# Kernel optimization log

Hardware: AMD Instinct MI355X
Metric: run time of the kernel (lower is better)

The kernel has to match this reference:

```python
import jax, jax.numpy as jnp
import numpy as np

B, V, L, C, H = 2, 8, 256, 1024, 16

def setup_inputs() -> dict:
    key = jax.random.key(0)
    ks = jax.random.split(key, 6)
    s = 0.02  # init scale for weights
    x = jax.random.normal(ks[0], (B, V, L, C), jnp.float32)
    Wq = jax.random.normal(ks[1], (C, C), jnp.float32) * s
    Wk = jax.random.normal(ks[2], (C, C), jnp.float32) * s
    Wv = jax.random.normal(ks[3], (C, C), jnp.float32) * s
    Wp = jax.random.normal(ks[4], (C, C), jnp.float32) * s
    bp = jnp.zeros((C,), jnp.float32)
    return {"x": x, "Wq": Wq, "Wk": Wk, "Wv": Wv, "Wp": Wp, "bp": bp}

def _view_mask(V, L):
    # view-level allow mask, expanded to token level [S, S]
    vi = jnp.arange(V)
    qv, kv = vi[:, None], vi[None, :]
    cross = ((qv == 0) & (kv == 1)) | ((qv == 1) & (kv == 0))
    later = (qv > 1) | (kv > 1)
    allow = cross | (later & (qv >= kv))  # [V, V]
    return jnp.repeat(jnp.repeat(allow, L, axis=0), L, axis=1)  # [V*L, V*L]

def reference(x, Wq, Wk, Wv, Wp, bp):
    b, v, l, c = x.shape
    h = H
    dh = c // h
    scale = dh ** -0.5
    s = v * l
    xf = x.reshape(b, s, c)
    # torch Linear: y = x @ W.T
    q = (xf @ Wq.T).reshape(b, s, h, dh).transpose(0, 2, 1, 3)  # [b,h,s,dh]
    k = (xf @ Wk.T).reshape(b, s, h, dh).transpose(0, 2, 1, 3)
    vv = (xf @ Wv.T).reshape(b, s, h, dh).transpose(0, 2, 1, 3)
    scores = jnp.einsum('bhqd,bhkd->bhqk', q, k) * scale  # [b,h,s,s]
    mask = _view_mask(v, l)
    scores = jnp.where(mask, scores, -jnp.inf)
    attn = jax.nn.softmax(scores, axis=-1)
    out = jnp.einsum('bhqk,bhkd->bhqd', attn, vv)
    out = out.transpose(0, 2, 1, 3).reshape(b, v, l, c)
    return out @ Wp.T + bp
```

## Files before the change

kernel.cpp:

```cpp
#include <hip/hip_runtime.h>
#include <stdint.h>

typedef unsigned short ushort_t;
typedef __attribute__((ext_vector_type(8))) __bf16 bf16x8;
typedef __attribute__((ext_vector_type(4))) float floatx4;
typedef __attribute__((ext_vector_type(2))) uint32_t uint32x2;

__device__ __forceinline__ ushort_t f2bf(float f) {
    uint32_t u = __builtin_bit_cast(uint32_t, f);
    u += 0x7fffu + ((u >> 16) & 1u);
    return (ushort_t)(u >> 16);
}

typedef __attribute__((address_space(1))) const void glb_void;
typedef __attribute__((address_space(3))) void lds_void;
__device__ __forceinline__ void gld16(const void* g, void* l) {
    __builtin_amdgcn_global_load_lds((glb_void*)g, (lds_void*)l, 16, 0, 0);
}

#define QSCALE 0.18033688011112042f

__global__ void cast_kernel(const float* __restrict__ x,
                            const float* __restrict__ Wq, const float* __restrict__ Wk,
                            const float* __restrict__ Wv, const float* __restrict__ Wp,
                            ushort_t* __restrict__ xb, ushort_t* __restrict__ Wqkvb,
                            ushort_t* __restrict__ Wpb)
{
    const int64_t NX = 4194304, NW = 1048576;
    int64_t i4 = ((int64_t)blockIdx.x * blockDim.x + threadIdx.x) * 4;
    const float* src; ushort_t* dst; int64_t off;
    if (i4 < NX)            { src = x;  dst = xb;          off = i4; }
    else if (i4 < NX+NW)    { src = Wq; dst = Wqkvb;       off = i4 - NX; }
    else if (i4 < NX+2*NW)  { src = Wk; dst = Wqkvb + NW;  off = i4 - NX - NW; }
    else if (i4 < NX+3*NW)  { src = Wv; dst = Wqkvb + 2*NW;off = i4 - NX - 2*NW; }
    else                    { src = Wp; dst = Wpb;         off = i4 - NX - 3*NW; }
    float4 v = *(const float4*)(src + off);
    ushort4 o;
    o.x = f2bf(v.x); o.y = f2bf(v.y); o.z = f2bf(v.z); o.w = f2bf(v.w);
    *(ushort4*)(dst + off) = o;
}

template<int BM, int BN, int BK, int MODE>
__global__ __launch_bounds__(256, 3)
void gemm_bt(const ushort_t* __restrict__ A, const ushort_t* __restrict__ Bmat,
             int M, int N, int K,
             ushort_t* __restrict__ qb, ushort_t* __restrict__ kb, ushort_t* __restrict__ vtb,
             float* __restrict__ outf, const float* __restrict__ bias)
{
    constexpr int KB32 = BK / 32;
    constexpr int NA = (BM / 16) * KB32;
    constexpr int NB = (BN / 16) * KB32;
    constexpr int NS = (NA + NB) / 4;
    constexpr int MT = BM / 32;
    constexpr int NTW = BN / 32;
    __shared__ ushort_t As[BM * BK];
    __shared__ ushort_t Bs[BN * BK];
    const int tid  = threadIdx.x;
    const int lane = tid & 63;
    const int wave = tid >> 6;
    const int m0 = blockIdx.x * BM;
    const int n0 = blockIdx.y * BN;
    const int wrow = (wave >> 1) * (BM / 2);
    const int wcol = (wave & 1) * (BN / 2);
    const int q_ = lane >> 4;
    const int ml = lane & 15;
    (void)M;

    floatx4 acc[MT][NTW];
    #pragma unroll
    for (int i = 0; i < MT; i++)
        #pragma unroll
        for (int j = 0; j < NTW; j++) acc[i][j] = floatx4{0.f,0.f,0.f,0.f};

    const int row_l = lane >> 2;
    const int col_l = (lane & 3) * 8;
    const ushort_t* gptr[NS];
    ushort_t* lptr[NS];
    #pragma unroll
    for (int i = 0; i < NS; i++) {
        int id = wave * NS + i;
        if (id < NA) {
            int rg = id / KB32, ch = id % KB32;
            gptr[i] = A + (int64_t)(m0 + rg*16 + row_l) * K + ch*32 + col_l;
            lptr[i] = As + id * 512;
        } else {
            int id2 = id - NA;
            int rg = id2 / KB32, ch = id2 % KB32;
            gptr[i] = Bmat + (int64_t)(n0 + rg*16 + row_l) * K + ch*32 + col_l;
            lptr[i] = Bs + id2 * 512;
        }
    }

    for (int k0 = 0; k0 < K; k0 += BK) {
        __syncthreads();
        #pragma unroll
        for (int i = 0; i < NS; i++) gld16(gptr[i] + k0, lptr[i]);
        __syncthreads();
        #pragma unroll
        for (int kk = 0; kk < KB32; kk++) {
            bf16x8 af[MT], bf[NTW];
            #pragma unroll
            for (int mt = 0; mt < MT; mt++)
                af[mt] = *(const bf16x8*)(As + ((wrow/16 + mt)*KB32 + kk)*512 + ml*32 + q_*8);
            #pragma unroll
            for (int nt = 0; nt < NTW; nt++)
                bf[nt] = *(const bf16x8*)(Bs + ((wcol/16 + nt)*KB32 + kk)*512 + ml*32 + q_*8);
            #pragma unroll
            for (int mt = 0; mt < MT; mt++)
                #pragma unroll
                for (int nt = 0; nt < NTW; nt++)
                    acc[mt][nt] = __builtin_amdgcn_mfma_f32_16x16x32_bf16(af[mt], bf[nt], acc[mt][nt], 0, 0, 0);
        }
    }

    if (MODE == 0) {
        #pragma unroll
        for (int mt = 0; mt < MT; mt++)
            #pragma unroll
            for (int nt = 0; nt < NTW; nt++) {
                floatx4 v = acc[mt][nt];
                int col = n0 + wcol + nt*16 + ml;
                int which = col >> 10;
                int nn = col & 1023;
                int h = nn >> 6, d = nn & 63;
                if (which < 2) {
                    ushort_t* dst = (which == 0) ? qb : kb;
                    float sc = (which == 0) ? QSCALE : 1.0f;
                    for (int r = 0; r < 4; r++) {
                        int rowg = m0 + wrow + mt*16 + q_*4 + r;
                        int b = rowg >> 11, s = rowg & 2047;
                        dst[(((int64_t)(b*16 + h) * 2048 + s) << 6) + d] = f2bf(v[r] * sc);
                    }
                } else {
                    int rowg0 = m0 + wrow + mt*16 + q_*4;
                    int b = rowg0 >> 11, sbase = rowg0 & 2047;
                    ushort4 o;
                    o.x = f2bf(v[0]); o.y = f2bf(v[1]); o.z = f2bf(v[2]); o.w = f2bf(v[3]);
                    *(ushort4*)(vtb + (((int64_t)(b*16 + h) * 64 + d) << 11) + sbase) = o;
                }
            }
    } else {
        #pragma unroll
        for (int mt = 0; mt < MT; mt++)
            #pragma unroll
            for (int nt = 0; nt < NTW; nt++) {
                floatx4 v = acc[mt][nt];
                int col = n0 + wcol + nt*16 + ml;
                float bv = bias[col];
                for (int r = 0; r < 4; r++) {
                    int rowg = m0 + wrow + mt*16 + q_*4 + r;
                    outf[(int64_t)rowg * N + col] = v[r] + bv;
                }
            }
    }
}

__global__ __launch_bounds__(256, 3)
void attn_kernel(const ushort_t* __restrict__ Q, const ushort_t* __restrict__ Kb,
                 const ushort_t* __restrict__ Vt, ushort_t* __restrict__ Out)
{
    __shared__ ushort_t Kl[8192];
    __shared__ ushort_t Vl[8192];
    __shared__ ushort_t Pl[4 * 16 * 136];

    int bi = blockIdx.x;
    int bh = (bi & 7) + 8 * ((bi >> 3) & 3);
    int qt = (bi >> 5) & 3;
    int qv = 7 - (bi >> 7);
    int b = bh >> 4, h = bh & 15;
    int tid = threadIdx.x;
    int wave = tid >> 6, lane = tid & 63;
    int q_ = lane >> 4, ml = lane & 15;
    int rlane = lane & 15, clane = lane >> 4;
    int s0 = qv*256 + qt*64 + wave*16;

    const ushort_t* Kbh = Kb + ((int64_t)bh << 17);
    const ushort_t* Vbh = Vt + ((int64_t)bh << 17);
    ushort_t* Pw = Pl + wave * (16 * 136);

    const ushort_t* Qp = Q + (((int64_t)bh*2048 + s0 + ml) << 6) + q_*8;
    bf16x8 aq0 = *(const bf16x8*)(Qp);
    bf16x8 aq1 = *(const bf16x8*)(Qp + 32);

    floatx4 o_acc[4];
    for (int i = 0; i < 4; i++) o_acc[i] = floatx4{0.f,0.f,0.f,0.f};
    float lsum = 0.f;

    const int nviews = (qv < 2) ? 1 : (qv + 1);
    const int vfix = qv ^ 1;

    for (int vi = 0; vi < nviews; vi++) {
        int kb0 = ((nviews == 1) ? vfix : vi) * 256;
        for (int ck = 0; ck < 2; ck++) {
            int koff = kb0 + ck * 128;

            __syncthreads();
            #pragma unroll
            for (int i = 0; i < 4; i++) {
                int id = wave*4 + i;
                const ushort_t* gk = Kbh + (((int64_t)(koff + (id >> 1)*16 + rlane)) << 6)
                                         + (id & 1)*32 + clane*8;
                gld16(gk, Kl + id*512);
                const ushort_t* gv = Vbh + ((int64_t)((id & 3)*16 + rlane) << 11)
                                         + koff + (id >> 2)*32 + clane*8;
                gld16(gv, Vl + id*512);
            }
            __syncthreads();

            #pragma unroll
            for (int kt = 0; kt < 8; kt++) {
                bf16x8 k0 = *(const bf16x8*)(Kl + kt*1024 + lane*8);
                bf16x8 k1 = *(const bf16x8*)(Kl + kt*1024 + 512 + lane*8);
                floatx4 cz = floatx4{0.f,0.f,0.f,0.f};
                cz = __builtin_amdgcn_mfma_f32_16x16x32_bf16(k0, aq0, cz, 0, 0, 0);
                cz = __builtin_amdgcn_mfma_f32_16x16x32_bf16(k1, aq1, cz, 0, 0, 0);

                float p0 = __builtin_amdgcn_exp2f(cz[0]);
                float p1 = __builtin_amdgcn_exp2f(cz[1]);
                float p2 = __builtin_amdgcn_exp2f(cz[2]);
                float p3 = __builtin_amdgcn_exp2f(cz[3]);
                lsum += (p0 + p1) + (p2 + p3);
                uint32x2 wv;
                wv[0] = (uint32_t)f2bf(p0) | ((uint32_t)f2bf(p1) << 16);
                wv[1] = (uint32_t)f2bf(p2) | ((uint32_t)f2bf(p3) << 16);
                *(uint32x2*)(Pw + ml*136 + kt*16 + q_*4) = wv;
            }

            asm volatile("s_waitcnt lgkmcnt(0)" ::: "memory");

            #pragma unroll
            for (int g = 0; g < 4; g++) {
                bf16x8 ap = *(const bf16x8*)(Pw + ml*136 + g*32 + q_*8);
                #pragma unroll
                for (int dt = 0; dt < 4; dt++) {
                    bf16x8 vv = *(const bf16x8*)(Vl + (g*4 + dt)*512 + lane*8);
                    o_acc[dt] = __builtin_amdgcn_mfma_f32_16x16x32_bf16(ap, vv, o_acc[dt], 0, 0, 0);
                }
            }
        }
    }

    lsum += __shfl_xor(lsum, 16);
    lsum += __shfl_xor(lsum, 32);
    float rinv[4];
    #pragma unroll
    for (int r = 0; r < 4; r++)
        rinv[r] = 1.0f / __shfl(lsum, q_*4 + r);

    #pragma unroll
    for (int dt = 0; dt < 4; dt++)
        #pragma unroll
        for (int r = 0; r < 4; r++) {
            float v = o_acc[dt][r] * rinv[r];
            int sr = s0 + q_*4 + r;
            Out[((int64_t)b*2048 + sr) * 1024 + h*64 + dt*16 + ml] = f2bf(v);
        }
}

extern "C" void kernel_launch(void* const* d_in, const int* in_sizes, int n_in,
                              void* d_out, int out_size, void* d_ws, size_t ws_size,
                              hipStream_t stream) {
    const float* x  = (const float*)d_in[0];
    const float* Wq = (const float*)d_in[1];
    const float* Wk = (const float*)d_in[2];
    const float* Wv = (const float*)d_in[3];
    const float* Wp = (const float*)d_in[4];
    const float* bp = (const float*)d_in[5];
    float* out = (float*)d_out;

    char* ws = (char*)d_ws;
    ushort_t* xb    = (ushort_t*)(ws);
    ushort_t* Wqkvb = (ushort_t*)(ws + ((size_t)8  << 20));
    ushort_t* Wpb   = (ushort_t*)(ws + ((size_t)14 << 20));
    ushort_t* qb    = (ushort_t*)(ws + ((size_t)16 << 20));
    ushort_t* kbuf  = (ushort_t*)(ws + ((size_t)24 << 20));
    ushort_t* vtb   = (ushort_t*)(ws + ((size_t)40 << 20));
    ushort_t* attno = xb;

    cast_kernel<<<8192, 256, 0, stream>>>(x, Wq, Wk, Wv, Wp, xb, Wqkvb, Wpb);

    gemm_bt<128,128,64,0><<<dim3(32, 24), 256, 0, stream>>>(
        xb, Wqkvb, 4096, 3072, 1024, qb, kbuf, vtb, nullptr, nullptr);

    attn_kernel<<<1024, 256, 0, stream>>>(qb, kbuf, vtb, attno);

    gemm_bt<128,64,64,1><<<dim3(32, 16), 256, 0, stream>>>(
        attno, Wpb, 4096, 1024, 1024, nullptr, nullptr, nullptr, out, bp);
}
```

Before: 173.3 us.

## Double-buffer K/V tiles in attention with async prefetch of next chunk

Replaces the single 128-key K/V LDS tile with two 64-key buffers. The next chunk's global-to-LDS loads are issued before computing on the current chunk, with vmcnt waits and raw s_barrier in place of the two __syncthreads per chunk. The goal is to hide global load latency behind the QK/softmax/PV MFMA work and shrink LDS per block. The trade-off is twice as many chunk iterations and barriers, plus reliance on hand-tuned waitcnt values for correctness.

```diff
diff --git a/kernel.cpp b/kernel.cpp
--- a/kernel.cpp
+++ b/kernel.cpp
@@ -159,9 +159,9 @@
 void attn_kernel(const ushort_t* __restrict__ Q, const ushort_t* __restrict__ Kb,
                  const ushort_t* __restrict__ Vt, ushort_t* __restrict__ Out)
 {
-    __shared__ ushort_t Kl[8192];
-    __shared__ ushort_t Vl[8192];
-    __shared__ ushort_t Pl[4 * 16 * 136];
+    __shared__ ushort_t Kd[2][4096];
+    __shared__ ushort_t Vd[2][4096];
+    __shared__ ushort_t Pl[4 * 16 * 72];
 
     int bi = blockIdx.x;
     int bh = (bi & 7) + 8 * ((bi >> 3) & 3);
@@ -176,7 +176,7 @@
 
     const ushort_t* Kbh = Kb + ((int64_t)bh << 17);
     const ushort_t* Vbh = Vt + ((int64_t)bh << 17);
-    ushort_t* Pw = Pl + wave * (16 * 136);
+    ushort_t* Pw = Pl + wave * (16 * 72);
 
     const ushort_t* Qp = Q + (((int64_t)bh*2048 + s0 + ml) << 6) + q_*8;
     bf16x8 aq0 = *(const bf16x8*)(Qp);
@@ -187,55 +187,78 @@
     float lsum = 0.f;
 
     const int nviews = (qv < 2) ? 1 : (qv + 1);
+    const int NC = nviews * 4;
     const int vfix = qv ^ 1;
 
-    for (int vi = 0; vi < nviews; vi++) {
-        int kb0 = ((nviews == 1) ? vfix : vi) * 256;
-        for (int ck = 0; ck < 2; ck++) {
-            int koff = kb0 + ck * 128;
-
-            __syncthreads();
-            #pragma unroll
-            for (int i = 0; i < 4; i++) {
-                int id = wave*4 + i;
-                const ushort_t* gk = Kbh + (((int64_t)(koff + (id >> 1)*16 + rlane)) << 6)
+    const int idA = wave*2, idB = wave*2 + 1;
+
+    {
+        int koff = ((nviews == 1) ? vfix : 0) * 256;
+        #pragma unroll
+        for (int i = 0; i < 2; i++) {
+            int id = idA + i;
+            const ushort_t* gk = Kbh + (((int64_t)(koff + (id >> 1)*16 + rlane)) << 6)
+                                     + (id & 1)*32 + clane*8;
+            gld16(gk, Kd[0] + id*512);
+            const ushort_t* gv = Vbh + ((int64_t)((id & 3)*16 + rlane) << 11)
+                                     + koff + (id >> 2)*32 + clane*8;
+            gld16(gv, Vd[0] + id*512);
+        }
+    }
+
+    for (int c = 0; c < NC; ++c) {
+        int cur = c & 1;
+        if (c > 0) __builtin_amdgcn_s_barrier();
+
+        if (c + 1 < NC) {
+            int koff_n = ((nviews == 1) ? vfix : ((c + 1) >> 2)) * 256 + ((c + 1) & 3) * 64;
+            #pragma unroll
+            for (int i = 0; i < 2; i++) {
+                int id = idA + i;
+                const ushort_t* gk = Kbh + (((int64_t)(koff_n + (id >> 1)*16 + rlane)) << 6)
                                          + (id & 1)*32 + clane*8;
-                gld16(gk, Kl + id*512);
+                gld16(gk, Kd[cur ^ 1] + id*512);
                 const ushort_t* gv = Vbh + ((int64_t)((id & 3)*16 + rlane) << 11)
-                                         + koff + (id >> 2)*32 + clane*8;
-                gld16(gv, Vl + id*512);
+                                         + koff_n + (id >> 2)*32 + clane*8;
+                gld16(gv, Vd[cur ^ 1] + id*512);
             }
-            __syncthreads();
-
-            #pragma unroll
-            for (int kt = 0; kt < 8; kt++) {
-                bf16x8 k0 = *(const bf16x8*)(Kl + kt*1024 + lane*8);
-                bf16x8 k1 = *(const bf16x8*)(Kl + kt*1024 + 512 + lane*8);
-                floatx4 cz = floatx4{0.f,0.f,0.f,0.f};
-                cz = __builtin_amdgcn_mfma_f32_16x16x32_bf16(k0, aq0, cz, 0, 0, 0);
-                cz = __builtin_amdgcn_mfma_f32_16x16x32_bf16(k1, aq1, cz, 0, 0, 0);
-
-                float p0 = __builtin_amdgcn_exp2f(cz[0]);
-                float p1 = __builtin_amdgcn_exp2f(cz[1]);
-                float p2 = __builtin_amdgcn_exp2f(cz[2]);
-                float p3 = __builtin_amdgcn_exp2f(cz[3]);
-                lsum += (p0 + p1) + (p2 + p3);
-                uint32x2 wv;
-                wv[0] = (uint32_t)f2bf(p0) | ((uint32_t)f2bf(p1) << 16);
-                wv[1] = (uint32_t)f2bf(p2) | ((uint32_t)f2bf(p3) << 16);
-                *(uint32x2*)(Pw + ml*136 + kt*16 + q_*4) = wv;
-            }
-
-            asm volatile("s_waitcnt lgkmcnt(0)" ::: "memory");
-
-            #pragma unroll
-            for (int g = 0; g < 4; g++) {
-                bf16x8 ap = *(const bf16x8*)(Pw + ml*136 + g*32 + q_*8);
-                #pragma unroll
-                for (int dt = 0; dt < 4; dt++) {
-                    bf16x8 vv = *(const bf16x8*)(Vl + (g*4 + dt)*512 + lane*8);
-                    o_acc[dt] = __builtin_amdgcn_mfma_f32_16x16x32_bf16(ap, vv, o_acc[dt], 0, 0, 0);
-                }
+            asm volatile("s_waitcnt vmcnt(4)" ::: "memory");
+        } else {
+            asm volatile("s_waitcnt vmcnt(0)" ::: "memory");
+        }
+        __builtin_amdgcn_s_barrier();
+
+        const ushort_t* Klc = Kd[cur];
+        const ushort_t* Vlc = Vd[cur];
+
+        #pragma unroll
+        for (int kt = 0; kt < 4; kt++) {
+            bf16x8 k0 = *(const bf16x8*)(Klc + kt*1024 + lane*8);
+            bf16x8 k1 = *(const bf16x8*)(Klc + kt*1024 + 512 + lane*8);
+            floatx4 cz = floatx4{0.f,0.f,0.f,0.f};
+            cz = __builtin_amdgcn_mfma_f32_16x16x32_bf16(k0, aq0, cz, 0, 0, 0);
+            cz = __builtin_amdgcn_mfma_f32_16x16x32_bf16(k1, aq1, cz, 0, 0, 0);
+
+            float p0 = __builtin_amdgcn_exp2f(cz[0]);
+            float p1 = __builtin_amdgcn_exp2f(cz[1]);
+            float p2 = __builtin_amdgcn_exp2f(cz[2]);
+            float p3 = __builtin_amdgcn_exp2f(cz[3]);
+            lsum += (p0 + p1) + (p2 + p3);
+            uint32x2 wv;
+            wv[0] = (uint32_t)f2bf(p0) | ((uint32_t)f2bf(p1) << 16);
+            wv[1] = (uint32_t)f2bf(p2) | ((uint32_t)f2bf(p3) << 16);
+            *(uint32x2*)(Pw + ml*72 + kt*16 + q_*4) = wv;
+        }
+
+        asm volatile("s_waitcnt lgkmcnt(0)" ::: "memory");
+
+        #pragma unroll
+        for (int g = 0; g < 2; g++) {
+            bf16x8 ap = *(const bf16x8*)(Pw + ml*72 + g*32 + q_*8);
+            #pragma unroll
+            for (int dt = 0; dt < 4; dt++) {
+                bf16x8 vv = *(const bf16x8*)(Vlc + (g*4 + dt)*512 + lane*8);
+                o_acc[dt] = __builtin_amdgcn_mfma_f32_16x16x32_bf16(ap, vv, o_acc[dt], 0, 0, 0);
             }
         }
     }
```

Result: slower. 177.8 us (+2.6%).
